# Kernel tuning notes

Hardware: AMD Instinct MI355X
Metric: run time of the kernel (lower is better)

## Reference

```python
import jax, jax.numpy as jnp
import numpy as np

BN_EPS = 1e-5
# regular 3x3 kernel grid offsets: row0 = dy, row1 = dx, kernel positions in row-major order
REG = jnp.array([[-1, -1, -1, 0, 0, 0, 1, 1, 1],
                 [-1,  0,  1, -1, 0, 1, -1, 0, 1]], dtype=jnp.float32)


def conv3x3(x, w, b):
    y = jax.lax.conv_general_dilated(x, w, window_strides=(1, 1),
                                     padding=((1, 1), (1, 1)),
                                     dimension_numbers=('NCHW', 'OIHW', 'NCHW'))
    return y + b[None, :, None, None]


def deform_conv3x3(x, dy, dx, w):
    # x: [N,C,H,W]; dy,dx: [N,9,H,W] per-kernel-tap offsets; w: [O,C,3,3]
    N, C, H, W = x.shape
    K = 9
    ky = jnp.repeat(jnp.arange(3), 3)   # [0,0,0,1,1,1,2,2,2]
    kx = jnp.tile(jnp.arange(3), 3)     # [0,1,2,0,1,2,0,1,2]
    # sampling positions: p = p_out - pad + k*dilation + offset (stride=1, pad=dil=1)
    py = dy + (jnp.arange(H) - 1)[None, None, :, None] + ky[None, :, None, None].astype(x.dtype)
    px = dx + (jnp.arange(W) - 1)[None, None, None, :] + kx[None, :, None, None].astype(x.dtype)
    y0 = jnp.floor(py)
    x0 = jnp.floor(px)
    wy = py - y0  # bilinear weights
    wx = px - x0
    y0i = y0.astype(jnp.int32)
    x0i = x0.astype(jnp.int32)
    nidx = jnp.arange(N)[:, None, None, None]

    def gather(yi, xi):
        valid = ((yi >= 0) & (yi < H) & (xi >= 0) & (xi < W)).astype(x.dtype)
        v = x[nidx, :, jnp.clip(yi, 0, H - 1), jnp.clip(xi, 0, W - 1)]  # [N,K,H,W,C]
        return v * valid[..., None]

    sampled = (gather(y0i,     x0i)     * ((1 - wy) * (1 - wx))[..., None]
             + gather(y0i,     x0i + 1) * ((1 - wy) * wx)[..., None]
             + gather(y0i + 1, x0i)     * (wy * (1 - wx))[..., None]
             + gather(y0i + 1, x0i + 1) * (wy * wx)[..., None])  # [N,K,H,W,C]
    O = w.shape[0]
    return jnp.einsum('nkhwc,ock->nohw', sampled, w.reshape(O, C, K))


def setup_inputs() -> dict:
    key = jax.random.key(0)
    ks = jax.random.split(key, 12)
    N, C, H, W = 2, 256, 96, 96
    O = 256
    sc = 1.0 / np.sqrt(C * 9)
    return {
        'x': jax.random.normal(ks[0], (N, C, H, W), jnp.float32),
        'mask_attention': jax.random.normal(ks[1], (N, C, H, W), jnp.float32),
        'w_tm': jax.random.normal(ks[2], (4, C, 3, 3), jnp.float32) * sc,
        'b_tm': jax.random.normal(ks[3], (4,), jnp.float32) * 0.01,
        'w_tr': jax.random.normal(ks[4], (2, C, 3, 3), jnp.float32) * sc,
        'b_tr': jax.random.normal(ks[5], (2,), jnp.float32) * 0.01,
        'w_deform': jax.random.normal(ks[6], (O, C, 3, 3), jnp.float32) * sc,
        'bn_gamma': jnp.ones((O,), jnp.float32),
        'bn_beta': jnp.zeros((O,), jnp.float32),
        'bn_mean': jax.random.normal(ks[7], (O,), jnp.float32) * 0.01,
        'bn_var': jax.random.uniform(ks[8], (O,), jnp.float32, 0.5, 1.5),
    }


def reference(x, mask_attention, w_tm, b_tm, w_tr, b_tr, w_deform,
              bn_gamma, bn_beta, bn_mean, bn_var):
    # mask_attention is overwritten by x in the original forward; ignored.
    N, C, H, W = x.shape
    tm = conv3x3(x, w_tm, b_tm)                       # [N,4,H,W]
    T = tm.transpose(0, 2, 3, 1).reshape(N, H, W, 2, 2)
    off = jnp.einsum('nhwij,jk->nhwik', T, REG) - REG  # [N,H,W,2,9], (T-I)@REG
    tr = conv3x3(x, w_tr, b_tr)                        # [N,2,H,W]
    off = off + tr.transpose(0, 2, 3, 1)[..., None]    # broadcast translation to all 9 taps
    dy = off[..., 0, :].transpose(0, 3, 1, 2)          # [N,9,H,W]
    dx = off[..., 1, :].transpose(0, 3, 1, 2)
    out = deform_conv3x3(x, dy, dx, w_deform)          # [N,O,H,W]
    inv = jax.lax.rsqrt(bn_var + BN_EPS)
    out = (out - bn_mean[None, :, None, None]) * (inv * bn_gamma)[None, :, None, None] \
          + bn_beta[None, :, None, None]
    return jax.nn.relu(out + x)
```

## Files before the change

kernel.cpp:

```cpp
#include <hip/hip_runtime.h>
#include <stdint.h>

#define H_ 96
#define W_ 96
#define C_ 256
#define O_ 256
#define N_ 2
#define HW_ (H_*W_)
#define M_ (N_*HW_)
#define GK 2304

typedef __bf16 bf16x8 __attribute__((ext_vector_type(8)));
typedef float f32x4 __attribute__((ext_vector_type(4)));
typedef unsigned short us4 __attribute__((ext_vector_type(4)));
typedef unsigned short us8 __attribute__((ext_vector_type(8)));

__device__ __forceinline__ unsigned short f2bf(float f) {
  union { float f; unsigned int u; } v; v.f = f;
  unsigned int u = v.u;
  return (unsigned short)((u + 0x7fffu + ((u >> 16) & 1u)) >> 16);
}
__device__ __forceinline__ float bf2f(unsigned short h) {
  union { unsigned int u; float f; } v; v.u = ((unsigned int)h) << 16;
  return v.f;
}

__global__ __launch_bounds__(256) void k_pre(const float* __restrict__ x,
                                             const float* __restrict__ w_df,
                                             const float* __restrict__ w_tm,
                                             const float* __restrict__ w_tr,
                                             unsigned short* __restrict__ xt,
                                             unsigned short* __restrict__ wfrag,
                                             unsigned short* __restrict__ w6p) {
  const int b = blockIdx.x;
  const int tid = threadIdx.x;
  if (b < 288) {
    __shared__ unsigned short tile[128][130];
    const int pt = b % 72;
    const int ch = (b / 72) & 1;
    const int n  = b / 144;
    const int p0 = pt * 128, c0 = ch * 128;
    const float* xp = x + (size_t)n * C_ * HW_;
    unsigned short* xtp = xt + (size_t)n * C_ * HW_;
    const int tx = tid & 31, ty = tid >> 5;
#pragma unroll
    for (int pass = 0; pass < 16; pass++) {
      const int c = pass * 8 + ty;
      const f32x4 v = *(const f32x4*)(xp + (size_t)(c0 + c) * HW_ + p0 + tx * 4);
#pragma unroll
      for (int i = 0; i < 4; i++) tile[tx * 4 + i][c] = f2bf(v[i]);
    }
    __syncthreads();
    const int wave = tid >> 6, lane = tid & 63;
    const int l32 = lane & 31, ph = lane >> 5;
#pragma unroll
    for (int pass = 0; pass < 16; pass++) {
      const int p = pass * 8 + wave * 2 + ph;
      us4 v;
#pragma unroll
      for (int i = 0; i < 4; i++) v[i] = tile[p][l32 * 4 + i];
      *(us4*)(xtp + (size_t)(p0 + p) * C_ + c0 + l32 * 4) = v;
    }
  } else if (b < 576) {
    const int base = (b - 288) * 2048 + tid * 8;
    const int l  = (base >> 3) & 63;
    const int g  = (base >> 9) & 15;
    const int ks = (base >> 13) & 7;
    const int t  = base >> 16;
    const int o  = g * 16 + (l & 15);
    const int c  = ks * 32 + (l >> 4) * 8;
    us8 res;
#pragma unroll
    for (int j = 0; j < 8; j++) res[j] = f2bf(w_df[(size_t)(o * 256 + c + j) * 9 + t]);
    *(us8*)(wfrag + base) = res;
  } else {
    int idx = (b - 576) * 256 + tid;
    int t = idx >> 12;
    int r = idx & 4095;
    int j = r >> 8;
    int c = r & 255;
    float v = 0.f;
    if (j < 4) v = w_tm[(size_t)(j * C_ + c) * 9 + t];
    else if (j < 6) v = w_tr[(size_t)((j - 4) * C_ + c) * 9 + t];
    w6p[idx] = f2bf(v);
  }
}

__global__ __launch_bounds__(256, 3) void k_fused(const unsigned short* __restrict__ xt,
                                                  const unsigned short* __restrict__ Wfrag,
                                                  const unsigned short* __restrict__ w6p,
                                                  const float* __restrict__ b_tm,
                                                  const float* __restrict__ b_tr,
                                                  const float* __restrict__ xres,
                                                  const float* __restrict__ gamma,
                                                  const float* __restrict__ beta,
                                                  const float* __restrict__ mean,
                                                  const float* __restrict__ var,
                                                  float* __restrict__ out) {
  __shared__ unsigned short As[2][32 * 256] __attribute__((aligned(16)));
  __shared__ float sred[4][16][8];
  __shared__ float coords_s[32][9][2];
  const int tid = threadIdx.x;
  const int wave = tid >> 6, lane = tid & 63;
  const int row = lane & 15, quad = lane >> 4;
  const int bm = (blockIdx.x & 7) * 72 + (blockIdx.x >> 3);
  const int m0 = bm * 32;
  const int n = m0 / HW_;
  const int sr = tid >> 4;
  const int cg = tid & 15;

  {
    const int hw0 = m0 - n * HW_;
    const int h = hw0 / W_;
    const int w0 = hw0 - h * W_;
    const int rh = wave >> 1;
    const int cq = (wave & 1) * 128;
    f32x4 oacc = {0.f, 0.f, 0.f, 0.f};
    const bf16x8 zero8 = {};
#pragma unroll
    for (int t = 0; t < 9; t++) {
      const int ty = t / 3, tx = t % 3;
      const int y = h + ty - 1;
      if (y < 0 || y >= H_) continue;
      const int xx = w0 + rh * 16 + row + tx - 1;
      const bool valid = (xx >= 0) && (xx < W_);
      const int xc = min(max(xx, 0), W_ - 1);
      const unsigned short* arow =
          xt + (size_t)((n * H_ + y) * W_ + xc) * C_ + cq + quad * 8;
      const unsigned short* brow =
          w6p + (size_t)(t * 16 + row) * C_ + cq + quad * 8;
#pragma unroll
      for (int ks = 0; ks < 4; ks++) {
        bf16x8 av = *(const bf16x8*)(const void*)(arow + ks * 32);
        if (!valid) av = zero8;
        bf16x8 bv = *(const bf16x8*)(const void*)(brow + ks * 32);
        oacc = __builtin_amdgcn_mfma_f32_16x16x32_bf16(av, bv, oacc, 0, 0, 0);
      }
    }
    if (row < 6) {
#pragma unroll
      for (int r = 0; r < 4; r++) sred[wave][quad * 4 + r][row] = oacc[r];
    }
  }
  __syncthreads();
  if (wave < 2 && lane < 16) {
    const int rg = wave * 16 + lane;
    const int hwm = m0 + rg - n * HW_;
    const int h = hwm / W_, w = hwm - h * W_;
    float a[6];
#pragma unroll
    for (int j = 0; j < 6; j++)
      a[j] = sred[wave * 2][lane][j] + sred[wave * 2 + 1][lane][j];
    const float tm0 = a[0] + b_tm[0];
    const float tm1 = a[1] + b_tm[1];
    const float tm2 = a[2] + b_tm[2];
    const float tm3 = a[3] + b_tm[3];
    const float tr0 = a[4] + b_tr[0];
    const float tr1 = a[5] + b_tr[1];
#pragma unroll
    for (int t = 0; t < 9; t++) {
      const float ry = (float)(t / 3) - 1.f;
      const float rx = (float)(t % 3) - 1.f;
      coords_s[rg][t][0] = (float)h + tr0 + tm0 * ry + tm1 * rx;
      coords_s[rg][t][1] = (float)w + tr1 + tm2 * ry + tm3 * rx;
    }
  }
  __syncthreads();

  f32x4 acc0[4] = {}, acc1[4] = {};
  float cwA[4], cwB[4];
  int cbA[4], cbB[4];
  us8 uA0[4], uA1[4], uB0[4], uB1[4];

#define PREP1(TAP, R, CW, CB)                                                  \
  {                                                                            \
    const float py = coords_s[R][TAP][0];                                      \
    const float px = coords_s[R][TAP][1];                                      \
    const float fy = floorf(py), fx = floorf(px);                              \
    const float wy = py - fy, wx = px - fx;                                    \
    const int y0 = (int)fy, x0 = (int)fx;                                      \
    const int y1 = y0 + 1, x1 = x0 + 1;                                        \
    const float vy0 = (y0 >= 0 && y0 < H_) ? 1.f : 0.f;                        \
    const float vy1 = (y1 >= 0 && y1 < H_) ? 1.f : 0.f;                        \
    const float vx0 = (x0 >= 0 && x0 < W_) ? 1.f : 0.f;                        \
    const float vx1 = (x1 >= 0 && x1 < W_) ? 1.f : 0.f;                        \
    CW[0] = (1.f - wy) * (1.f - wx) * vy0 * vx0;                               \
    CW[1] = (1.f - wy) * wx * vy0 * vx1;                                       \
    CW[2] = wy * (1.f - wx) * vy1 * vx0;                                       \
    CW[3] = wy * wx * vy1 * vx1;                                               \
    const int cy0 = min(max(y0, 0), H_ - 1), cy1 = min(max(y1, 0), H_ - 1);    \
    const int cx0 = min(max(x0, 0), W_ - 1), cx1 = min(max(x1, 0), W_ - 1);    \
    CB[0] = ((n * H_ + cy0) * W_ + cx0) * C_;                                  \
    CB[1] = ((n * H_ + cy0) * W_ + cx1) * C_;                                  \
    CB[2] = ((n * H_ + cy1) * W_ + cx0) * C_;                                  \
    CB[3] = ((n * H_ + cy1) * W_ + cx1) * C_;                                  \
  }

#define LOADC1(CB, U0, U1)                                                     \
  {                                                                            \
    const int cc = cg * 16;                                                    \
    U0[0] = *(const us8*)(xt + CB[0] + cc); U1[0] = *(const us8*)(xt + CB[0] + cc + 8); \
    U0[1] = *(const us8*)(xt + CB[1] + cc); U1[1] = *(const us8*)(xt + CB[1] + cc + 8); \
    U0[2] = *(const us8*)(xt + CB[2] + cc); U1[2] = *(const us8*)(xt + CB[2] + cc + 8); \
    U0[3] = *(const us8*)(xt + CB[3] + cc); U1[3] = *(const us8*)(xt + CB[3] + cc + 8); \
  }

#define LERP8(DST, U, CW)                                                      \
  {                                                                            \
    _Pragma("unroll")                                                          \
    for (int e = 0; e < 8; e++)                                                \
      DST[e] = f2bf(CW[0] * bf2f(U[0][e]) + CW[1] * bf2f(U[1][e]) +            \
                    CW[2] * bf2f(U[2][e]) + CW[3] * bf2f(U[3][e]));            \
  }

  PREP1(0, sr, cwA, cbA);
  PREP1(0, sr + 16, cwB, cbB);
  LOADC1(cbA, uA0, uA1);
  LOADC1(cbB, uB0, uB1);

  for (int tap = 0; tap < 9; tap++) {
    unsigned short* __restrict__ asb = As[tap & 1];
    {
      const int q0 = cg * 2, q1 = cg * 2 + 1;
      const int s0 = (q0 & 24) | ((q0 ^ sr) & 7);
      const int s1 = (q1 & 24) | ((q1 ^ sr) & 7);
      us8 r0, r1;
      LERP8(r0, uA0, cwA);
      LERP8(r1, uA1, cwA);
      *(us8*)(void*)&asb[sr * 256 + s0 * 8] = r0;
      *(us8*)(void*)&asb[sr * 256 + s1 * 8] = r1;
      LERP8(r0, uB0, cwB);
      LERP8(r1, uB1, cwB);
      *(us8*)(void*)&asb[(sr + 16) * 256 + s0 * 8] = r0;
      *(us8*)(void*)&asb[(sr + 16) * 256 + s1 * 8] = r1;
    }

    const unsigned short* wfTap =
        Wfrag + (size_t)(tap * 8) * 8192 + wave * 2048 + lane * 8;
    bf16x8 bv[4];
#pragma unroll
    for (int ot = 0; ot < 4; ot++) bv[ot] = *(const bf16x8*)(const void*)(wfTap + ot * 512);

    __syncthreads();

    if (tap < 8) {
      PREP1(tap + 1, sr, cwA, cbA);
      PREP1(tap + 1, sr + 16, cwB, cbB);
      LOADC1(cbA, uA0, uA1);
      LOADC1(cbB, uB0, uB1);
    }

#pragma unroll
    for (int ks = 0; ks < 8; ks++) {
      const int q = ks * 4 + quad;
      const int slot = (q & 24) | ((q ^ row) & 7);
      const bf16x8 av0 = *(const bf16x8*)(const void*)&asb[row * 256 + slot * 8];
      const bf16x8 av1 = *(const bf16x8*)(const void*)&asb[(row + 16) * 256 + slot * 8];
      bf16x8 bn[4];
      if (ks < 7) {
        const unsigned short* wfn = wfTap + (size_t)(ks + 1) * 8192;
#pragma unroll
        for (int ot = 0; ot < 4; ot++) bn[ot] = *(const bf16x8*)(const void*)(wfn + ot * 512);
      }
#pragma unroll
      for (int ot = 0; ot < 4; ot++)
        acc0[ot] = __builtin_amdgcn_mfma_f32_16x16x32_bf16(av0, bv[ot], acc0[ot], 0, 0, 0);
#pragma unroll
      for (int ot = 0; ot < 4; ot++)
        acc1[ot] = __builtin_amdgcn_mfma_f32_16x16x32_bf16(av1, bv[ot], acc1[ot], 0, 0, 0);
      if (ks < 7) {
#pragma unroll
        for (int ot = 0; ot < 4; ot++) bv[ot] = bn[ot];
      }
    }
  }

  const int hwb = m0 - n * HW_ + quad * 4;
#pragma unroll
  for (int ot = 0; ot < 4; ot++) {
    const int o = wave * 64 + ot * 16 + row;
    const float sc = rsqrtf(var[o] + 1e-5f) * gamma[o];
    const float bi = beta[o] - mean[o] * sc;
    const size_t ob0 = (size_t)(n * O_ + o) * HW_ + hwb;
    f32x4 rv = *(const f32x4*)(xres + ob0);
    f32x4 ov;
#pragma unroll
    for (int r = 0; r < 4; r++) ov[r] = fmaxf(acc0[ot][r] * sc + bi + rv[r], 0.f);
    *(f32x4*)(out + ob0) = ov;
    const size_t ob1 = ob0 + 16;
    rv = *(const f32x4*)(xres + ob1);
#pragma unroll
    for (int r = 0; r < 4; r++) ov[r] = fmaxf(acc1[ot][r] * sc + bi + rv[r], 0.f);
    *(f32x4*)(out + ob1) = ov;
  }
}

extern "C" void kernel_launch(void* const* d_in, const int* in_sizes, int n_in,
                              void* d_out, int out_size, void* d_ws, size_t ws_size,
                              hipStream_t stream) {
  const float* x     = (const float*)d_in[0];
  const float* w_tm  = (const float*)d_in[2];
  const float* b_tm  = (const float*)d_in[3];
  const float* w_tr  = (const float*)d_in[4];
  const float* b_tr  = (const float*)d_in[5];
  const float* w_df  = (const float*)d_in[6];
  const float* gamma = (const float*)d_in[7];
  const float* beta  = (const float*)d_in[8];
  const float* mean  = (const float*)d_in[9];
  const float* var   = (const float*)d_in[10];
  float* out = (float*)d_out;

  char* ws = (char*)d_ws;
  unsigned short* xt    = (unsigned short*)(ws);
  unsigned short* wfrag = (unsigned short*)(ws + 9437184);
  unsigned short* w6p   = (unsigned short*)(ws + 9437184 + 1179648);

  k_pre<<<720, 256, 0, stream>>>(x, w_df, w_tm, w_tr, xt, wfrag, w6p);
  k_fused<<<576, 256, 0, stream>>>(xt, wfrag, w6p, b_tm, b_tr, x,
                                   gamma, beta, mean, var, out);
}
```

Measured before the change: 177.7 us.

## Double block to 512 threads, split gather rows and output channels across waves

The fused deform-conv kernel now runs 8 waves per block instead of 4. Each thread gathers and interpolates one row instead of two, each wave owns 32 output channels instead of 64, and the offset-conv reduction is split four ways. The bilinear interpolation is also vectorised to unpack bf16 pairs and convert with native bf16 casts. The aim is more latency hiding for the gather loads and less work per thread on the critical path. The cost is higher block-level synchronisation and a tighter register budget under launch_bounds(512,4).

```diff
diff --git a/kernel.cpp b/kernel.cpp
--- a/kernel.cpp
+++ b/kernel.cpp
@@ -12,6 +12,7 @@
 
 typedef __bf16 bf16x8 __attribute__((ext_vector_type(8)));
 typedef float f32x4 __attribute__((ext_vector_type(4)));
+typedef float f32x2 __attribute__((ext_vector_type(2)));
 typedef unsigned short us4 __attribute__((ext_vector_type(4)));
 typedef unsigned short us8 __attribute__((ext_vector_type(8)));
 
@@ -23,6 +24,13 @@
 __device__ __forceinline__ float bf2f(unsigned short h) {
   union { unsigned int u; float f; } v; v.u = ((unsigned int)h) << 16;
   return v.f;
+}
+__device__ __forceinline__ f32x2 bfpair(unsigned int a) {
+  union { unsigned int u; float f; } lo, hi;
+  lo.u = a << 16;
+  hi.u = a & 0xffff0000u;
+  f32x2 r; r[0] = lo.f; r[1] = hi.f;
+  return r;
 }
 
 __global__ __launch_bounds__(256) void k_pre(const float* __restrict__ x,
@@ -86,7 +94,7 @@
   }
 }
 
-__global__ __launch_bounds__(256, 3) void k_fused(const unsigned short* __restrict__ xt,
+__global__ __launch_bounds__(512, 4) void k_fused(const unsigned short* __restrict__ xt,
                                                   const unsigned short* __restrict__ Wfrag,
                                                   const unsigned short* __restrict__ w6p,
                                                   const float* __restrict__ b_tm,
@@ -98,7 +106,7 @@
                                                   const float* __restrict__ var,
                                                   float* __restrict__ out) {
   __shared__ unsigned short As[2][32 * 256] __attribute__((aligned(16)));
-  __shared__ float sred[4][16][8];
+  __shared__ float sred[8][16][8];
   __shared__ float coords_s[32][9][2];
   const int tid = threadIdx.x;
   const int wave = tid >> 6, lane = tid & 63;
@@ -113,8 +121,8 @@
     const int hw0 = m0 - n * HW_;
     const int h = hw0 / W_;
     const int w0 = hw0 - h * W_;
-    const int rh = wave >> 1;
-    const int cq = (wave & 1) * 128;
+    const int rh = wave >> 2;
+    const int cq = (wave & 3) * 64;
     f32x4 oacc = {0.f, 0.f, 0.f, 0.f};
     const bf16x8 zero8 = {};
 #pragma unroll
@@ -130,7 +138,7 @@
       const unsigned short* brow =
           w6p + (size_t)(t * 16 + row) * C_ + cq + quad * 8;
 #pragma unroll
-      for (int ks = 0; ks < 4; ks++) {
+      for (int ks = 0; ks < 2; ks++) {
         bf16x8 av = *(const bf16x8*)(const void*)(arow + ks * 32);
         if (!valid) av = zero8;
         bf16x8 bv = *(const bf16x8*)(const void*)(brow + ks * 32);
@@ -150,7 +158,8 @@
     float a[6];
 #pragma unroll
     for (int j = 0; j < 6; j++)
-      a[j] = sred[wave * 2][lane][j] + sred[wave * 2 + 1][lane][j];
+      a[j] = sred[wave * 4 + 0][lane][j] + sred[wave * 4 + 1][lane][j] +
+             sred[wave * 4 + 2][lane][j] + sred[wave * 4 + 3][lane][j];
     const float tm0 = a[0] + b_tm[0];
     const float tm1 = a[1] + b_tm[1];
     const float tm2 = a[2] + b_tm[2];
@@ -167,15 +176,15 @@
   }
   __syncthreads();
 
-  f32x4 acc0[4] = {}, acc1[4] = {};
-  float cwA[4], cwB[4];
-  int cbA[4], cbB[4];
-  us8 uA0[4], uA1[4], uB0[4], uB1[4];
-
-#define PREP1(TAP, R, CW, CB)                                                  \
+  f32x4 acc0[2] = {}, acc1[2] = {};
+  float cw[4];
+  int cb[4];
+  us8 u0[4], u1[4];
+
+#define PREP1(TAP)                                                             \
   {                                                                            \
-    const float py = coords_s[R][TAP][0];                                      \
-    const float px = coords_s[R][TAP][1];                                      \
+    const float py = coords_s[sr][TAP][0];                                     \
+    const float px = coords_s[sr][TAP][1];                                     \
     const float fy = floorf(py), fx = floorf(px);                              \
     const float wy = py - fy, wx = px - fx;                                    \
     const int y0 = (int)fy, x0 = (int)fx;                                      \
@@ -184,39 +193,44 @@
     const float vy1 = (y1 >= 0 && y1 < H_) ? 1.f : 0.f;                        \
     const float vx0 = (x0 >= 0 && x0 < W_) ? 1.f : 0.f;                        \
     const float vx1 = (x1 >= 0 && x1 < W_) ? 1.f : 0.f;                        \
-    CW[0] = (1.f - wy) * (1.f - wx) * vy0 * vx0;                               \
-    CW[1] = (1.f - wy) * wx * vy0 * vx1;                                       \
-    CW[2] = wy * (1.f - wx) * vy1 * vx0;                                       \
-    CW[3] = wy * wx * vy1 * vx1;                                               \
+    cw[0] = (1.f - wy) * (1.f - wx) * vy0 * vx0;                               \
+    cw[1] = (1.f - wy) * wx * vy0 * vx1;                                       \
+    cw[2] = wy * (1.f - wx) * vy1 * vx0;                                       \
+    cw[3] = wy * wx * vy1 * vx1;                                               \
     const int cy0 = min(max(y0, 0), H_ - 1), cy1 = min(max(y1, 0), H_ - 1);    \
     const int cx0 = min(max(x0, 0), W_ - 1), cx1 = min(max(x1, 0), W_ - 1);    \
-    CB[0] = ((n * H_ + cy0) * W_ + cx0) * C_;                                  \
-    CB[1] = ((n * H_ + cy0) * W_ + cx1) * C_;                                  \
-    CB[2] = ((n * H_ + cy1) * W_ + cx0) * C_;                                  \
-    CB[3] = ((n * H_ + cy1) * W_ + cx1) * C_;                                  \
-  }
-
-#define LOADC1(CB, U0, U1)                                                     \
+    cb[0] = ((n * H_ + cy0) * W_ + cx0) * C_;                                  \
+    cb[1] = ((n * H_ + cy0) * W_ + cx1) * C_;                                  \
+    cb[2] = ((n * H_ + cy1) * W_ + cx0) * C_;                                  \
+    cb[3] = ((n * H_ + cy1) * W_ + cx1) * C_;                                  \
+  }
+
+#define LOADC1()                                                               \
   {                                                                            \
     const int cc = cg * 16;                                                    \
-    U0[0] = *(const us8*)(xt + CB[0] + cc); U1[0] = *(const us8*)(xt + CB[0] + cc + 8); \
-    U0[1] = *(const us8*)(xt + CB[1] + cc); U1[1] = *(const us8*)(xt + CB[1] + cc + 8); \
-    U0[2] = *(const us8*)(xt + CB[2] + cc); U1[2] = *(const us8*)(xt + CB[2] + cc + 8); \
-    U0[3] = *(const us8*)(xt + CB[3] + cc); U1[3] = *(const us8*)(xt + CB[3] + cc + 8); \
-  }
-
-#define LERP8(DST, U, CW)                                                      \
+    u0[0] = *(const us8*)(xt + cb[0] + cc); u1[0] = *(const us8*)(xt + cb[0] + cc + 8); \
+    u0[1] = *(const us8*)(xt + cb[1] + cc); u1[1] = *(const us8*)(xt + cb[1] + cc + 8); \
+    u0[2] = *(const us8*)(xt + cb[2] + cc); u1[2] = *(const us8*)(xt + cb[2] + cc + 8); \
+    u0[3] = *(const us8*)(xt + cb[3] + cc); u1[3] = *(const us8*)(xt + cb[3] + cc + 8); \
+  }
+
+#define LERP8V(DST, U)                                                         \
   {                                                                            \
+    const unsigned int* a0 = (const unsigned int*)&U[0];                       \
+    const unsigned int* a1 = (const unsigned int*)&U[1];                       \
+    const unsigned int* a2 = (const unsigned int*)&U[2];                       \
+    const unsigned int* a3 = (const unsigned int*)&U[3];                       \
     _Pragma("unroll")                                                          \
-    for (int e = 0; e < 8; e++)                                                \
-      DST[e] = f2bf(CW[0] * bf2f(U[0][e]) + CW[1] * bf2f(U[1][e]) +            \
-                    CW[2] * bf2f(U[2][e]) + CW[3] * bf2f(U[3][e]));            \
-  }
-
-  PREP1(0, sr, cwA, cbA);
-  PREP1(0, sr + 16, cwB, cbB);
-  LOADC1(cbA, uA0, uA1);
-  LOADC1(cbB, uB0, uB1);
+    for (int p = 0; p < 4; p++) {                                              \
+      f32x2 acc = bfpair(a0[p]) * cw[0] + bfpair(a1[p]) * cw[1] +              \
+                  bfpair(a2[p]) * cw[2] + bfpair(a3[p]) * cw[3];               \
+      DST[p * 2]     = (__bf16)acc[0];                                         \
+      DST[p * 2 + 1] = (__bf16)acc[1];                                         \
+    }                                                                          \
+  }
+
+  PREP1(0);
+  LOADC1();
 
   for (int tap = 0; tap < 9; tap++) {
     unsigned short* __restrict__ asb = As[tap & 1];
@@ -224,30 +238,24 @@
       const int q0 = cg * 2, q1 = cg * 2 + 1;
       const int s0 = (q0 & 24) | ((q0 ^ sr) & 7);
       const int s1 = (q1 & 24) | ((q1 ^ sr) & 7);
-      us8 r0, r1;
-      LERP8(r0, uA0, cwA);
-      LERP8(r1, uA1, cwA);
-      *(us8*)(void*)&asb[sr * 256 + s0 * 8] = r0;
-      *(us8*)(void*)&asb[sr * 256 + s1 * 8] = r1;
-      LERP8(r0, uB0, cwB);
-      LERP8(r1, uB1, cwB);
-      *(us8*)(void*)&asb[(sr + 16) * 256 + s0 * 8] = r0;
-      *(us8*)(void*)&asb[(sr + 16) * 256 + s1 * 8] = r1;
+      bf16x8 r0, r1;
+      LERP8V(r0, u0);
+      LERP8V(r1, u1);
+      *(bf16x8*)(void*)&asb[sr * 256 + s0 * 8] = r0;
+      *(bf16x8*)(void*)&asb[sr * 256 + s1 * 8] = r1;
     }
 
     const unsigned short* wfTap =
-        Wfrag + (size_t)(tap * 8) * 8192 + wave * 2048 + lane * 8;
-    bf16x8 bv[4];
-#pragma unroll
-    for (int ot = 0; ot < 4; ot++) bv[ot] = *(const bf16x8*)(const void*)(wfTap + ot * 512);
+        Wfrag + (size_t)(tap * 8) * 8192 + wave * 1024 + lane * 8;
+    bf16x8 bv[2];
+#pragma unroll
+    for (int ot = 0; ot < 2; ot++) bv[ot] = *(const bf16x8*)(const void*)(wfTap + ot * 512);
 
     __syncthreads();
 
     if (tap < 8) {
-      PREP1(tap + 1, sr, cwA, cbA);
-      PREP1(tap + 1, sr + 16, cwB, cbB);
-      LOADC1(cbA, uA0, uA1);
-      LOADC1(cbB, uB0, uB1);
+      PREP1(tap + 1);
+      LOADC1();
     }
 
 #pragma unroll
@@ -256,29 +264,29 @@
       const int slot = (q & 24) | ((q ^ row) & 7);
       const bf16x8 av0 = *(const bf16x8*)(const void*)&asb[row * 256 + slot * 8];
       const bf16x8 av1 = *(const bf16x8*)(const void*)&asb[(row + 16) * 256 + slot * 8];
-      bf16x8 bn[4];
+      bf16x8 bn[2];
       if (ks < 7) {
         const unsigned short* wfn = wfTap + (size_t)(ks + 1) * 8192;
 #pragma unroll
-        for (int ot = 0; ot < 4; ot++) bn[ot] = *(const bf16x8*)(const void*)(wfn + ot * 512);
+        for (int ot = 0; ot < 2; ot++) bn[ot] = *(const bf16x8*)(const void*)(wfn + ot * 512);
       }
 #pragma unroll
-      for (int ot = 0; ot < 4; ot++)
+      for (int ot = 0; ot < 2; ot++)
         acc0[ot] = __builtin_amdgcn_mfma_f32_16x16x32_bf16(av0, bv[ot], acc0[ot], 0, 0, 0);
 #pragma unroll
-      for (int ot = 0; ot < 4; ot++)
+      for (int ot = 0; ot < 2; ot++)
         acc1[ot] = __builtin_amdgcn_mfma_f32_16x16x32_bf16(av1, bv[ot], acc1[ot], 0, 0, 0);
       if (ks < 7) {
 #pragma unroll
-        for (int ot = 0; ot < 4; ot++) bv[ot] = bn[ot];
+        for (int ot = 0; ot < 2; ot++) bv[ot] = bn[ot];
       }
     }
   }
 
   const int hwb = m0 - n * HW_ + quad * 4;
 #pragma unroll
-  for (int ot = 0; ot < 4; ot++) {
-    const int o = wave * 64 + ot * 16 + row;
+  for (int ot = 0; ot < 2; ot++) {
+    const int o = wave * 32 + ot * 16 + row;
     const float sc = rsqrtf(var[o] + 1e-5f) * gamma[o];
     const float bi = beta[o] - mean[o] * sc;
     const size_t ob0 = (size_t)(n * O_ + o) * HW_ + hwb;
@@ -316,6 +324,6 @@
   unsigned short* w6p   = (unsigned short*)(ws + 9437184 + 1179648);
 
   k_pre<<<720, 256, 0, stream>>>(x, w_df, w_tm, w_tr, xt, wfrag, w6p);
-  k_fused<<<576, 256, 0, stream>>>(xt, wfrag, w6p, b_tm, b_tr, x,
+  k_fused<<<576, 512, 0, stream>>>(xt, wfrag, w6p, b_tm, b_tr, x,
                                    gamma, beta, mean, var, out);
 }
```

Result: no change. 177.1 us (-0.3%).
